# Optimization experiments

Hardware: AMD Instinct MI355X
Metric: run time of the kernel (lower is better)

The kernel has to match this reference:

```python
import jax, jax.numpy as jnp
import numpy as np

B, S, D, H = 2, 2048, 1024, 16
DH = D // H  # 64
NEG = -1000000000.0


def setup_inputs() -> dict:
    key = jax.random.key(0)
    ks = jax.random.split(key, 10)
    scale = 1.0 / np.sqrt(D)
    inp = {
        "x": jax.random.normal(ks[0], (B, S, D), dtype=jnp.float32),
        "mask": jax.random.randint(ks[1], (B, S, S), 0, 2, dtype=jnp.int32),
        "Wq": jax.random.normal(ks[2], (D, D), dtype=jnp.float32) * scale,
        "bq": jnp.zeros((D,), dtype=jnp.float32),
        "Wk": jax.random.normal(ks[3], (D, D), dtype=jnp.float32) * scale,
        "bk": jnp.zeros((D,), dtype=jnp.float32),
        "Wv": jax.random.normal(ks[4], (D, D), dtype=jnp.float32) * scale,
        "bv": jnp.zeros((D,), dtype=jnp.float32),
        "Wo": jax.random.normal(ks[5], (D, D), dtype=jnp.float32) * scale,
        "bo": jnp.zeros((D,), dtype=jnp.float32),
    }
    return inp


def reference(x, mask, Wq, bq, Wk, bk, Wv, bv, Wo, bo):
    b, s, _ = x.shape
    # Linear projections (torch Linear: y = x @ W^T + b), then split heads -> [b,h,s,dh]
    q = (x @ Wq.T + bq).reshape(b, s, H, DH).transpose(0, 2, 1, 3)
    k = (x @ Wk.T + bk).reshape(b, s, H, DH).transpose(0, 2, 1, 3)
    v = (x @ Wv.T + bv).reshape(b, s, H, DH).transpose(0, 2, 1, 3)
    # scores: [b,h,sq,sk]
    scores = jnp.einsum("bhqd,bhkd->bhqk", q, k) / jnp.sqrt(jnp.float32(DH))
    # code masks where mask == 0 (mask broadcast over heads)
    scores = jnp.where(mask[:, None, :, :] == 0, NEG, scores)
    attn = jax.nn.softmax(scores, axis=-1)
    out = jnp.einsum("bhqk,bhkd->bhqd", attn, v)  # [b,h,sq,dh]
    out = out.transpose(0, 2, 1, 3).reshape(b, s, D)  # merge heads -> [b,s,d]
    return out @ Wo.T + bo
```

## Files before the change

kernel.cpp:

```cpp
#include <hip/hip_runtime.h>
#include <stdint.h>

#define SB 2
#define SS 2048
#define SD 1024
#define SH 16
#define SDH 64
#define SM (SB*SS)
#define QSCALE 0.18033688011112043f

typedef __attribute__((ext_vector_type(8))) short short8;
typedef __attribute__((ext_vector_type(4))) short short4v;
typedef __attribute__((ext_vector_type(4))) float f32x4;
typedef __attribute__((ext_vector_type(4))) float float4v;
typedef __attribute__((ext_vector_type(4))) uint32_t uint4v;
typedef __attribute__((ext_vector_type(2))) unsigned long long ull2;

__device__ static inline short f2bf(float f) {
    uint32_t u = __float_as_uint(f);
    u += 0x7fffu + ((u >> 16) & 1u);
    return (short)(u >> 16);
}

__device__ static inline void gload_lds16(const void* g, void* l) {
    __builtin_amdgcn_global_load_lds(
        (__attribute__((address_space(1))) void*)g,
        (__attribute__((address_space(3))) void*)l,
        16, 0, 0);
}

#define NX4 (SM*SD/4)
#define NW4 (SD*SD/4)
#define NCVT (NX4 + 4*NW4)
#define NMSK (SB*SS*SS)
__global__ void prep_kernel(const float* __restrict__ x,
                            const float* __restrict__ Wq, const float* __restrict__ Wk,
                            const float* __restrict__ Wv, const float* __restrict__ Wo,
                            const int* __restrict__ mask,
                            short* __restrict__ xb,
                            short* __restrict__ wqb, short* __restrict__ wkb,
                            short* __restrict__ wvb, short* __restrict__ wob,
                            unsigned long long* __restrict__ bits) {
    unsigned i = blockIdx.x * 256u + threadIdx.x;
    if (i < NCVT) {
        const float* src; short* dst; unsigned idx;
        if (i < NX4) { src = x; dst = xb; idx = i; }
        else {
            unsigned j = i - NX4;
            unsigned sel = j >> 18;
            idx = j & (NW4 - 1);
            src = (sel == 0) ? Wq : (sel == 1) ? Wk : (sel == 2) ? Wv : Wo;
            dst = (sel == 0) ? wqb : (sel == 1) ? wkb : (sel == 2) ? wvb : wob;
        }
        float4v v = *(const float4v*)(src + (size_t)idx * 4);
        short4v o;
        o[0] = f2bf(v[0]); o[1] = f2bf(v[1]); o[2] = f2bf(v[2]); o[3] = f2bf(v[3]);
        *(short4v*)(dst + (size_t)idx * 4) = o;
    } else {
        unsigned j = i - NCVT;
        int pred = mask[j] != 0;
        unsigned long long bb = __ballot(pred);
        if ((threadIdx.x & 63u) == 0u) bits[j >> 6] = bb;
    }
}

__global__ __launch_bounds__(256, 3) void gemm_qkv_kernel(
    const short* __restrict__ A,
    const short* __restrict__ W0, const short* __restrict__ W1, const short* __restrict__ W2,
    const float* __restrict__ b0, const float* __restrict__ b1, const float* __restrict__ b2,
    short* __restrict__ O0, short* __restrict__ O1, short* __restrict__ O2) {
    unsigned flat = blockIdx.x + (blockIdx.y << 3) + (blockIdx.z << 8);
    unsigned swz = (flat & 7u) * 96u + (flat >> 3);
    const int bx = swz & 7, by = (swz >> 3) & 31, bz = swz >> 8;

    const short* W = (bz == 0) ? W0 : (bz == 1) ? W1 : W2;
    const float* bias = (bz == 0) ? b0 : (bz == 1) ? b1 : b2;
    short* C = (bz == 0) ? O0 : (bz == 1) ? O1 : O2;
    const float scale = (bz == 0) ? QSCALE : 1.0f;
    const int rowBase = by * 128, colBase = bx * 128;
    const int K = SD, N = SD;

    __shared__ short As[2][128 * 32];
    __shared__ short Bs[2][128 * 32];
    const int tid = threadIdx.x, lane = tid & 63, wid = tid >> 6;
    const int r15 = lane & 15, hi = lane >> 4;
    const int wr = wid >> 1, wc = wid & 1;

    const int chBase0 = wid * 64, chBase1 = 256 + wid * 64;
    const int ch0 = chBase0 + lane, ch1 = chBase1 + lane;
    const short* aP0 = A + (size_t)(rowBase + (ch0 >> 2)) * K + (ch0 & 3) * 8;
    const short* aP1 = A + (size_t)(rowBase + (ch1 >> 2)) * K + (ch1 & 3) * 8;
    const short* bP0 = W + (size_t)(colBase + (ch0 >> 2)) * K + (ch0 & 3) * 8;
    const short* bP1 = W + (size_t)(colBase + (ch1 >> 2)) * K + (ch1 & 3) * 8;

    gload_lds16(aP0, &As[0][chBase0 * 8]);
    gload_lds16(aP1, &As[0][chBase1 * 8]);
    gload_lds16(bP0, &Bs[0][chBase0 * 8]);
    gload_lds16(bP1, &Bs[0][chBase1 * 8]);

    f32x4 acc[4][4] = {};
    const int NIT = K / 32;

    for (int it = 0; it < NIT; ++it) {
        __syncthreads();
        const int cur = it & 1, nxt = cur ^ 1;
        if (it + 1 < NIT) {
            int kt = (it + 1) * 32;
            gload_lds16(aP0 + kt, &As[nxt][chBase0 * 8]);
            gload_lds16(aP1 + kt, &As[nxt][chBase1 * 8]);
            gload_lds16(bP0 + kt, &Bs[nxt][chBase0 * 8]);
            gload_lds16(bP1 + kt, &Bs[nxt][chBase1 * 8]);
        }

        short8 aF[4], bF[4];
#pragma unroll
        for (int mi = 0; mi < 4; ++mi)
            aF[mi] = *(const short8*)&As[cur][(wr * 64 + mi * 16 + r15) * 32 + hi * 8];
#pragma unroll
        for (int ni = 0; ni < 4; ++ni)
            bF[ni] = *(const short8*)&Bs[cur][(wc * 64 + ni * 16 + r15) * 32 + hi * 8];

        __builtin_amdgcn_s_setprio(1);
#pragma unroll
        for (int mi = 0; mi < 4; ++mi)
#pragma unroll
            for (int ni = 0; ni < 4; ++ni)
                acc[mi][ni] = __builtin_amdgcn_mfma_f32_16x16x32_bf16(aF[mi], bF[ni], acc[mi][ni], 0, 0, 0);
        __builtin_amdgcn_s_setprio(0);
    }

#pragma unroll
    for (int ni = 0; ni < 4; ++ni) {
        int col = colBase + wc * 64 + ni * 16 + r15;
        float bv = bias[col];
#pragma unroll
        for (int mi = 0; mi < 4; ++mi) {
#pragma unroll
            for (int r = 0; r < 4; ++r) {
                int row = rowBase + wr * 64 + mi * 16 + hi * 4 + r;
                C[(size_t)row * N + col] = f2bf((acc[mi][ni][r] + bv) * scale);
            }
        }
    }
}

__global__ __launch_bounds__(256, 2) void gemm_out_kernel(
    const short* __restrict__ A, const short* __restrict__ W,
    const float* __restrict__ bias, float* __restrict__ C) {
    unsigned flat = blockIdx.x + (blockIdx.y << 4);
    unsigned swz = (flat & 7u) * 64u + (flat >> 3);
    const int rowBase = ((swz >> 4) & 31) * 128, colBase = (swz & 15) * 64;
    const int K = SD, N = SD;

    __shared__ short As[2][128 * 32];
    __shared__ short Bs[2][64 * 32];
    const int tid = threadIdx.x, lane = tid & 63, wid = tid >> 6;
    const int r15 = lane & 15, hi = lane >> 4;

    const int chBase0 = wid * 64, chBase1 = 256 + wid * 64;
    const int ch0 = chBase0 + lane, ch1 = chBase1 + lane;
    const short* aP0 = A + (size_t)(rowBase + (ch0 >> 2)) * K + (ch0 & 3) * 8;
    const short* aP1 = A + (size_t)(rowBase + (ch1 >> 2)) * K + (ch1 & 3) * 8;
    const short* bP0 = W + (size_t)(colBase + (ch0 >> 2)) * K + (ch0 & 3) * 8;

    gload_lds16(aP0, &As[0][chBase0 * 8]);
    gload_lds16(aP1, &As[0][chBase1 * 8]);
    gload_lds16(bP0, &Bs[0][chBase0 * 8]);

    f32x4 acc[2][4] = {};
    const int NIT = K / 32;

    for (int it = 0; it < NIT; ++it) {
        __syncthreads();
        const int cur = it & 1, nxt = cur ^ 1;
        if (it + 1 < NIT) {
            int kt = (it + 1) * 32;
            gload_lds16(aP0 + kt, &As[nxt][chBase0 * 8]);
            gload_lds16(aP1 + kt, &As[nxt][chBase1 * 8]);
            gload_lds16(bP0 + kt, &Bs[nxt][chBase0 * 8]);
        }

        short8 aF[2], bF[4];
#pragma unroll
        for (int mi = 0; mi < 2; ++mi)
            aF[mi] = *(const short8*)&As[cur][(wid * 32 + mi * 16 + r15) * 32 + hi * 8];
#pragma unroll
        for (int ni = 0; ni < 4; ++ni)
            bF[ni] = *(const short8*)&Bs[cur][(ni * 16 + r15) * 32 + hi * 8];

        __builtin_amdgcn_s_setprio(1);
#pragma unroll
        for (int mi = 0; mi < 2; ++mi)
#pragma unroll
            for (int ni = 0; ni < 4; ++ni)
                acc[mi][ni] = __builtin_amdgcn_mfma_f32_16x16x32_bf16(aF[mi], bF[ni], acc[mi][ni], 0, 0, 0);
        __builtin_amdgcn_s_setprio(0);
    }

#pragma unroll
    for (int ni = 0; ni < 4; ++ni) {
        int col = colBase + ni * 16 + r15;
        float bv = bias[col];
#pragma unroll
        for (int mi = 0; mi < 2; ++mi) {
#pragma unroll
            for (int r = 0; r < 4; ++r) {
                int row = rowBase + wid * 32 + mi * 16 + hi * 4 + r;
                C[(size_t)row * N + col] = acc[mi][ni][r] + bv;
            }
        }
    }
}

__global__ __launch_bounds__(512, 4) void attn_kernel(
    const short* __restrict__ Q, const short* __restrict__ K, const short* __restrict__ V,
    const unsigned long long* __restrict__ mbits, short* __restrict__ O) {
    unsigned flat = blockIdx.x + (blockIdx.y << 4) + (blockIdx.z << 8);
    unsigned swz = (flat & 7u) * 64u + (flat >> 3);
    const int bx = swz & 15, h = (swz >> 4) & 15, b = swz >> 8;

    const int tid = threadIdx.x, lane = tid & 63, wid = tid >> 6;
    const int r15 = lane & 15, hi = lane >> 4;
    const int q0 = bx * 128 + wid * 16;
    const int brow = b * SS;

    __shared__ short Ks[2][128 * 64];
    __shared__ short Vt[2][64 * 136];

    const short* Kbase = K + (size_t)brow * SD + h * SDH;
    const short* Vbase = V + (size_t)brow * SD + h * SDH;
    const ull2* mrow_p = (const ull2*)(mbits + (size_t)(brow + q0 + r15) * (SS / 64));

    short8 qF[2];
#pragma unroll
    for (int kd = 0; kd < 2; ++kd)
        qF[kd] = *(const short8*)&Q[(size_t)(brow + q0 + r15) * SD + h * SDH + kd * 32 + hi * 8];

    short8 onesF;
#pragma unroll
    for (int j = 0; j < 8; ++j) onesF[j] = (short)0x3F80;

    f32x4 o[4] = {};
    f32x4 lacc = {};

    const int vp = tid & 63, vc0 = (tid >> 6) * 8;
    const int k2 = 2 * vp;
    const int vcol = (k2 & 96) | ((k2 & 12) << 1) | ((k2 & 16) >> 2) | (k2 & 3);
    const int sh4 = hi * 4;

#pragma unroll
    for (int c2 = 0; c2 < 2; ++c2) {
        int chBase = c2 * 512 + wid * 64;
        int ch = chBase + lane;
        int row = ch >> 3, c16 = ch & 7;
        gload_lds16(Kbase + (size_t)row * SD + ((c16 ^ (row & 7)) * 8), &Ks[0][chBase * 8]);
    }
    short8 va = *(const short8*)(Vbase + (size_t)k2 * SD + vc0);
    short8 vb2 = *(const short8*)(Vbase + (size_t)(k2 + 1) * SD + vc0);
    ull2 mb = mrow_p[0];
#pragma unroll
    for (int j = 0; j < 8; ++j) {
        uint32_t pk = (uint32_t)(uint16_t)va[j] | ((uint32_t)(uint16_t)vb2[j] << 16);
        *(uint32_t*)&Vt[0][(vc0 + j) * 136 + vcol] = pk;
    }

    const int NT = SS / 128;
    for (int t = 0; t < NT; ++t) {
        __syncthreads();
        const int cur = t & 1, nxt = cur ^ 1;
        const int tn = (t < NT - 1) ? t + 1 : t;

#pragma unroll
        for (int c2 = 0; c2 < 2; ++c2) {
            int chBase = c2 * 512 + wid * 64;
            int ch = chBase + lane;
            int row = ch >> 3, c16 = ch & 7;
            gload_lds16(Kbase + (size_t)(tn * 128 + row) * SD + ((c16 ^ (row & 7)) * 8),
                        &Ks[nxt][chBase * 8]);
        }
        va  = *(const short8*)(Vbase + (size_t)(tn * 128 + k2) * SD + vc0);
        vb2 = *(const short8*)(Vbase + (size_t)(tn * 128 + k2 + 1) * SD + vc0);
        ull2 mbn = mrow_p[tn];

        f32x4 s[8] = {};
        __builtin_amdgcn_s_setprio(1);
#pragma unroll
        for (int kc = 0; kc < 8; ++kc) {
            int krow = kc * 16 + r15;
#pragma unroll
            for (int kd = 0; kd < 2; ++kd) {
                short8 kF = *(const short8*)&Ks[cur][krow * 64 + (((kd * 4 + hi) ^ (krow & 7)) * 8)];
                s[kc] = __builtin_amdgcn_mfma_f32_16x16x32_bf16(kF, qF[kd], s[kc], 0, 0, 0);
            }
        }
        __builtin_amdgcn_s_setprio(0);

        {
            unsigned w0 = (unsigned)mb[0], w1 = (unsigned)(mb[0] >> 32);
            unsigned w2 = (unsigned)mb[1], w3 = (unsigned)(mb[1] >> 32);
            unsigned hsh[8] = { w0 >> sh4, (w0 >> 16) >> sh4, w1 >> sh4, (w1 >> 16) >> sh4,
                                w2 >> sh4, (w2 >> 16) >> sh4, w3 >> sh4, (w3 >> 16) >> sh4 };
#pragma unroll
            for (int kc = 0; kc < 8; ++kc) {
                unsigned hh = hsh[kc];
#pragma unroll
                for (int r = 0; r < 4; ++r) {
                    float e;
                    asm("v_exp_f32 %0, %1" : "=v"(e) : "v"(s[kc][r]));
                    int m = ((int)(hh << (31 - r))) >> 31;
                    s[kc][r] = __uint_as_float(__float_as_uint(e) & (unsigned)m);
                }
            }
        }

        short8 pF[4];
#pragma unroll
        for (int kf = 0; kf < 4; ++kf) {
            uint32_t w0, w1, w2, w3;
            asm("v_cvt_pk_bf16_f32 %0, %1, %2" : "=v"(w0) : "v"(s[2 * kf][0]),     "v"(s[2 * kf][1]));
            asm("v_cvt_pk_bf16_f32 %0, %1, %2" : "=v"(w1) : "v"(s[2 * kf][2]),     "v"(s[2 * kf][3]));
            asm("v_cvt_pk_bf16_f32 %0, %1, %2" : "=v"(w2) : "v"(s[2 * kf + 1][0]), "v"(s[2 * kf + 1][1]));
            asm("v_cvt_pk_bf16_f32 %0, %1, %2" : "=v"(w3) : "v"(s[2 * kf + 1][2]), "v"(s[2 * kf + 1][3]));
            uint4v t4 = { w0, w1, w2, w3 };
            pF[kf] = __builtin_bit_cast(short8, t4);
        }

        __builtin_amdgcn_s_setprio(1);
#pragma unroll
        for (int df = 0; df < 4; ++df) {
#pragma unroll
            for (int kf = 0; kf < 4; ++kf) {
                short8 vF = *(const short8*)&Vt[cur][(df * 16 + r15) * 136 + kf * 32 + hi * 8];
                o[df] = __builtin_amdgcn_mfma_f32_16x16x32_bf16(pF[kf], vF, o[df], 0, 0, 0);
            }
        }
#pragma unroll
        for (int kf = 0; kf < 4; ++kf)
            lacc = __builtin_amdgcn_mfma_f32_16x16x32_bf16(pF[kf], onesF, lacc, 0, 0, 0);
        __builtin_amdgcn_s_setprio(0);

#pragma unroll
        for (int j = 0; j < 8; ++j) {
            uint32_t pk = (uint32_t)(uint16_t)va[j] | ((uint32_t)(uint16_t)vb2[j] << 16);
            *(uint32_t*)&Vt[nxt][(vc0 + j) * 136 + vcol] = pk;
        }
        mb = mbn;
    }

#pragma unroll
    for (int r = 0; r < 4; ++r) {
        float inv = 1.0f / lacc[r];
        size_t row = (size_t)(brow + q0 + hi * 4 + r);
#pragma unroll
        for (int df = 0; df < 4; ++df)
            O[row * SD + h * SDH + df * 16 + r15] = f2bf(o[df][r] * inv);
    }
}

extern "C" void kernel_launch(void* const* d_in, const int* in_sizes, int n_in,
                              void* d_out, int out_size, void* d_ws, size_t ws_size,
                              hipStream_t stream) {
    const float* x  = (const float*)d_in[0];
    const int* mask = (const int*)d_in[1];
    const float* Wq = (const float*)d_in[2];
    const float* bq = (const float*)d_in[3];
    const float* Wk = (const float*)d_in[4];
    const float* bk = (const float*)d_in[5];
    const float* Wv = (const float*)d_in[6];
    const float* bv = (const float*)d_in[7];
    const float* Wo = (const float*)d_in[8];
    const float* bo = (const float*)d_in[9];
    float* out = (float*)d_out;

    char* ws = (char*)d_ws;
    size_t off = 0;
    auto alloc = [&](size_t bytes) { void* p = ws + off; off += (bytes + 255) & ~(size_t)255; return p; };

    short* xb  = (short*)alloc((size_t)SM * SD * 2);
    short* wqb = (short*)alloc((size_t)SD * SD * 2);
    short* wkb = (short*)alloc((size_t)SD * SD * 2);
    short* wvb = (short*)alloc((size_t)SD * SD * 2);
    short* wob = (short*)alloc((size_t)SD * SD * 2);
    short* Qb  = (short*)alloc((size_t)SM * SD * 2);
    short* Kb  = (short*)alloc((size_t)SM * SD * 2);
    short* Vb  = (short*)alloc((size_t)SM * SD * 2);
    short* AOb = (short*)alloc((size_t)SM * SD * 2);
    unsigned long long* mbits = (unsigned long long*)alloc((size_t)SB * SS * (SS / 64) * 8);

    prep_kernel<<<(NCVT + NMSK) / 256, 256, 0, stream>>>(
        x, Wq, Wk, Wv, Wo, mask, xb, wqb, wkb, wvb, wob, mbits);

    gemm_qkv_kernel<<<dim3(SD / 128, SM / 128, 3), 256, 0, stream>>>(
        xb, wqb, wkb, wvb, bq, bk, bv, Qb, Kb, Vb);

    attn_kernel<<<dim3(SS / 128, SH, SB), 512, 0, stream>>>(Qb, Kb, Vb, mbits, AOb);

    gemm_out_kernel<<<dim3(SD / 64, SM / 128), 256, 0, stream>>>(AOb, wob, bo, out);
}
```

Measured before the change: 132.6 us.

## Process two 16-row query tiles per wave in attention to reuse K/V fragments

Each wave now handles 32 query rows, as two 16-row sub-tiles, instead of 16. Each block covers 256 queries, so the grid halves and each K/V tile loaded into shared memory serves twice as many queries. Every LDS K and V fragment read now feeds two MFMAs. The cost is doubled accumulator and score registers per thread, so launch bounds drop to 2 blocks per CU with lower occupancy and fewer blocks (256) to spread over the CUs.

```diff
diff --git a/kernel.cpp b/kernel.cpp
--- a/kernel.cpp
+++ b/kernel.cpp
@@ -212,16 +212,16 @@
     }
 }
 
-__global__ __launch_bounds__(512, 4) void attn_kernel(
+__global__ __launch_bounds__(512, 2) void attn_kernel(
     const short* __restrict__ Q, const short* __restrict__ K, const short* __restrict__ V,
     const unsigned long long* __restrict__ mbits, short* __restrict__ O) {
-    unsigned flat = blockIdx.x + (blockIdx.y << 4) + (blockIdx.z << 8);
-    unsigned swz = (flat & 7u) * 64u + (flat >> 3);
-    const int bx = swz & 15, h = (swz >> 4) & 15, b = swz >> 8;
+    unsigned flat = blockIdx.x + (blockIdx.y << 3) + (blockIdx.z << 7);
+    unsigned swz = (flat & 7u) * 32u + (flat >> 3);
+    const int bx = swz & 7, h = (swz >> 3) & 15, b = swz >> 7;
 
     const int tid = threadIdx.x, lane = tid & 63, wid = tid >> 6;
     const int r15 = lane & 15, hi = lane >> 4;
-    const int q0 = bx * 128 + wid * 16;
+    const int q0 = bx * 256 + wid * 32;
     const int brow = b * SS;
 
     __shared__ short Ks[2][128 * 64];
@@ -229,19 +229,22 @@
 
     const short* Kbase = K + (size_t)brow * SD + h * SDH;
     const short* Vbase = V + (size_t)brow * SD + h * SDH;
-    const ull2* mrow_p = (const ull2*)(mbits + (size_t)(brow + q0 + r15) * (SS / 64));
-
-    short8 qF[2];
-#pragma unroll
-    for (int kd = 0; kd < 2; ++kd)
-        qF[kd] = *(const short8*)&Q[(size_t)(brow + q0 + r15) * SD + h * SDH + kd * 32 + hi * 8];
+    const ull2* mp0 = (const ull2*)(mbits + (size_t)(brow + q0 + r15) * (SS / 64));
+    const ull2* mp1 = (const ull2*)(mbits + (size_t)(brow + q0 + 16 + r15) * (SS / 64));
+
+    short8 qF[2][2];
+#pragma unroll
+    for (int c = 0; c < 2; ++c)
+#pragma unroll
+        for (int kd = 0; kd < 2; ++kd)
+            qF[c][kd] = *(const short8*)&Q[(size_t)(brow + q0 + c * 16 + r15) * SD + h * SDH + kd * 32 + hi * 8];
 
     short8 onesF;
 #pragma unroll
     for (int j = 0; j < 8; ++j) onesF[j] = (short)0x3F80;
 
-    f32x4 o[4] = {};
-    f32x4 lacc = {};
+    f32x4 o0[4] = {}, o1[4] = {};
+    f32x4 lacc0 = {}, lacc1 = {};
 
     const int vp = tid & 63, vc0 = (tid >> 6) * 8;
     const int k2 = 2 * vp;
@@ -257,7 +260,7 @@
     }
     short8 va = *(const short8*)(Vbase + (size_t)k2 * SD + vc0);
     short8 vb2 = *(const short8*)(Vbase + (size_t)(k2 + 1) * SD + vc0);
-    ull2 mb = mrow_p[0];
+    ull2 mb0 = mp0[0], mb1 = mp1[0];
 #pragma unroll
     for (int j = 0; j < 8; ++j) {
         uint32_t pk = (uint32_t)(uint16_t)va[j] | ((uint32_t)(uint16_t)vb2[j] << 16);
@@ -280,9 +283,9 @@
         }
         va  = *(const short8*)(Vbase + (size_t)(tn * 128 + k2) * SD + vc0);
         vb2 = *(const short8*)(Vbase + (size_t)(tn * 128 + k2 + 1) * SD + vc0);
-        ull2 mbn = mrow_p[tn];
-
-        f32x4 s[8] = {};
+        ull2 mbn0 = mp0[tn], mbn1 = mp1[tn];
+
+        f32x4 s0[8] = {}, s1[8] = {};
         __builtin_amdgcn_s_setprio(1);
 #pragma unroll
         for (int kc = 0; kc < 8; ++kc) {
@@ -290,14 +293,16 @@
 #pragma unroll
             for (int kd = 0; kd < 2; ++kd) {
                 short8 kF = *(const short8*)&Ks[cur][krow * 64 + (((kd * 4 + hi) ^ (krow & 7)) * 8)];
-                s[kc] = __builtin_amdgcn_mfma_f32_16x16x32_bf16(kF, qF[kd], s[kc], 0, 0, 0);
+                s0[kc] = __builtin_amdgcn_mfma_f32_16x16x32_bf16(kF, qF[0][kd], s0[kc], 0, 0, 0);
+                s1[kc] = __builtin_amdgcn_mfma_f32_16x16x32_bf16(kF, qF[1][kd], s1[kc], 0, 0, 0);
             }
         }
         __builtin_amdgcn_s_setprio(0);
 
+        short8 pF0[4], pF1[4];
         {
-            unsigned w0 = (unsigned)mb[0], w1 = (unsigned)(mb[0] >> 32);
-            unsigned w2 = (unsigned)mb[1], w3 = (unsigned)(mb[1] >> 32);
+            unsigned w0 = (unsigned)mb0[0], w1 = (unsigned)(mb0[0] >> 32);
+            unsigned w2 = (unsigned)mb0[1], w3 = (unsigned)(mb0[1] >> 32);
             unsigned hsh[8] = { w0 >> sh4, (w0 >> 16) >> sh4, w1 >> sh4, (w1 >> 16) >> sh4,
                                 w2 >> sh4, (w2 >> 16) >> sh4, w3 >> sh4, (w3 >> 16) >> sh4 };
 #pragma unroll
@@ -306,23 +311,48 @@
 #pragma unroll
                 for (int r = 0; r < 4; ++r) {
                     float e;
-                    asm("v_exp_f32 %0, %1" : "=v"(e) : "v"(s[kc][r]));
+                    asm("v_exp_f32 %0, %1" : "=v"(e) : "v"(s0[kc][r]));
                     int m = ((int)(hh << (31 - r))) >> 31;
-                    s[kc][r] = __uint_as_float(__float_as_uint(e) & (unsigned)m);
+                    s0[kc][r] = __uint_as_float(__float_as_uint(e) & (unsigned)m);
                 }
             }
-        }
-
-        short8 pF[4];
-#pragma unroll
-        for (int kf = 0; kf < 4; ++kf) {
-            uint32_t w0, w1, w2, w3;
-            asm("v_cvt_pk_bf16_f32 %0, %1, %2" : "=v"(w0) : "v"(s[2 * kf][0]),     "v"(s[2 * kf][1]));
-            asm("v_cvt_pk_bf16_f32 %0, %1, %2" : "=v"(w1) : "v"(s[2 * kf][2]),     "v"(s[2 * kf][3]));
-            asm("v_cvt_pk_bf16_f32 %0, %1, %2" : "=v"(w2) : "v"(s[2 * kf + 1][0]), "v"(s[2 * kf + 1][1]));
-            asm("v_cvt_pk_bf16_f32 %0, %1, %2" : "=v"(w3) : "v"(s[2 * kf + 1][2]), "v"(s[2 * kf + 1][3]));
-            uint4v t4 = { w0, w1, w2, w3 };
-            pF[kf] = __builtin_bit_cast(short8, t4);
+#pragma unroll
+            for (int kf = 0; kf < 4; ++kf) {
+                uint32_t a0, a1, a2, a3;
+                asm("v_cvt_pk_bf16_f32 %0, %1, %2" : "=v"(a0) : "v"(s0[2 * kf][0]),     "v"(s0[2 * kf][1]));
+                asm("v_cvt_pk_bf16_f32 %0, %1, %2" : "=v"(a1) : "v"(s0[2 * kf][2]),     "v"(s0[2 * kf][3]));
+                asm("v_cvt_pk_bf16_f32 %0, %1, %2" : "=v"(a2) : "v"(s0[2 * kf + 1][0]), "v"(s0[2 * kf + 1][1]));
+                asm("v_cvt_pk_bf16_f32 %0, %1, %2" : "=v"(a3) : "v"(s0[2 * kf + 1][2]), "v"(s0[2 * kf + 1][3]));
+                uint4v t4 = { a0, a1, a2, a3 };
+                pF0[kf] = __builtin_bit_cast(short8, t4);
+            }
+        }
+        {
+            unsigned w0 = (unsigned)mb1[0], w1 = (unsigned)(mb1[0] >> 32);
+            unsigned w2 = (unsigned)mb1[1], w3 = (unsigned)(mb1[1] >> 32);
+            unsigned hsh[8] = { w0 >> sh4, (w0 >> 16) >> sh4, w1 >> sh4, (w1 >> 16) >> sh4,
+                                w2 >> sh4, (w2 >> 16) >> sh4, w3 >> sh4, (w3 >> 16) >> sh4 };
+#pragma unroll
+            for (int kc = 0; kc < 8; ++kc) {
+                unsigned hh = hsh[kc];
+#pragma unroll
+                for (int r = 0; r < 4; ++r) {
+                    float e;
+                    asm("v_exp_f32 %0, %1" : "=v"(e) : "v"(s1[kc][r]));
+                    int m = ((int)(hh << (31 - r))) >> 31;
+                    s1[kc][r] = __uint_as_float(__float_as_uint(e) & (unsigned)m);
+                }
+            }
+#pragma unroll
+            for (int kf = 0; kf < 4; ++kf) {
+                uint32_t a0, a1, a2, a3;
+                asm("v_cvt_pk_bf16_f32 %0, %1, %2" : "=v"(a0) : "v"(s1[2 * kf][0]),     "v"(s1[2 * kf][1]));
+                asm("v_cvt_pk_bf16_f32 %0, %1, %2" : "=v"(a1) : "v"(s1[2 * kf][2]),     "v"(s1[2 * kf][3]));
+                asm("v_cvt_pk_bf16_f32 %0, %1, %2" : "=v"(a2) : "v"(s1[2 * kf + 1][0]), "v"(s1[2 * kf + 1][1]));
+                asm("v_cvt_pk_bf16_f32 %0, %1, %2" : "=v"(a3) : "v"(s1[2 * kf + 1][2]), "v"(s1[2 * kf + 1][3]));
+                uint4v t4 = { a0, a1, a2, a3 };
+                pF1[kf] = __builtin_bit_cast(short8, t4);
+            }
         }
 
         __builtin_amdgcn_s_setprio(1);
@@ -331,12 +361,15 @@
 #pragma unroll
             for (int kf = 0; kf < 4; ++kf) {
                 short8 vF = *(const short8*)&Vt[cur][(df * 16 + r15) * 136 + kf * 32 + hi * 8];
-                o[df] = __builtin_amdgcn_mfma_f32_16x16x32_bf16(pF[kf], vF, o[df], 0, 0, 0);
-            }
-        }
-#pragma unroll
-        for (int kf = 0; kf < 4; ++kf)
-            lacc = __builtin_amdgcn_mfma_f32_16x16x32_bf16(pF[kf], onesF, lacc, 0, 0, 0);
+                o0[df] = __builtin_amdgcn_mfma_f32_16x16x32_bf16(pF0[kf], vF, o0[df], 0, 0, 0);
+                o1[df] = __builtin_amdgcn_mfma_f32_16x16x32_bf16(pF1[kf], vF, o1[df], 0, 0, 0);
+            }
+        }
+#pragma unroll
+        for (int kf = 0; kf < 4; ++kf) {
+            lacc0 = __builtin_amdgcn_mfma_f32_16x16x32_bf16(pF0[kf], onesF, lacc0, 0, 0, 0);
+            lacc1 = __builtin_amdgcn_mfma_f32_16x16x32_bf16(pF1[kf], onesF, lacc1, 0, 0, 0);
+        }
         __builtin_amdgcn_s_setprio(0);
 
 #pragma unroll
@@ -344,16 +377,20 @@
             uint32_t pk = (uint32_t)(uint16_t)va[j] | ((uint32_t)(uint16_t)vb2[j] << 16);
             *(uint32_t*)&Vt[nxt][(vc0 + j) * 136 + vcol] = pk;
         }
-        mb = mbn;
+        mb0 = mbn0; mb1 = mbn1;
     }
 
 #pragma unroll
     for (int r = 0; r < 4; ++r) {
-        float inv = 1.0f / lacc[r];
-        size_t row = (size_t)(brow + q0 + hi * 4 + r);
-#pragma unroll
-        for (int df = 0; df < 4; ++df)
-            O[row * SD + h * SDH + df * 16 + r15] = f2bf(o[df][r] * inv);
+        float inv0 = 1.0f / lacc0[r];
+        float inv1 = 1.0f / lacc1[r];
+        size_t row0 = (size_t)(brow + q0 + hi * 4 + r);
+        size_t row1 = row0 + 16;
+#pragma unroll
+        for (int df = 0; df < 4; ++df) {
+            O[row0 * SD + h * SDH + df * 16 + r15] = f2bf(o0[df][r] * inv0);
+            O[row1 * SD + h * SDH + df * 16 + r15] = f2bf(o1[df][r] * inv1);
+        }
     }
 }
 
@@ -393,7 +430,7 @@
     gemm_qkv_kernel<<<dim3(SD / 128, SM / 128, 3), 256, 0, stream>>>(
         xb, wqb, wkb, wvb, bq, bk, bv, Qb, Kb, Vb);
 
-    attn_kernel<<<dim3(SS / 128, SH, SB), 512, 0, stream>>>(Qb, Kb, Vb, mbits, AOb);
+    attn_kernel<<<dim3(SS / 256, SH, SB), 512, 0, stream>>>(Qb, Kb, Vb, mbits, AOb);
 
     gemm_out_kernel<<<dim3(SD / 64, SM / 128), 256, 0, stream>>>(AOb, wob, bo, out);
 }
```

New measurement: 138.2 us. 1.04x slower.
